# Kernel optimization log

Measured on AMD Instinct MI355X. Metric: run time of the kernel, lower is better.

Reference implementation:

```python
import jax, jax.numpy as jnp
import numpy as np

FEATURE_DIM = 1024
HEAD_NUM = 16
HIDDEN_DIM = FEATURE_DIM // HEAD_NUM


def setup_inputs() -> dict:
    key = jax.random.key(0)
    ks = jax.random.split(key, 12)
    B, S, D = 4, 2048, FEATURE_DIM
    s = 1.0 / np.sqrt(D)
    inp = {
        "query": jax.random.normal(ks[0], (B, S, D), jnp.float32),
        "key": jax.random.normal(ks[1], (B, S, D), jnp.float32),
        "value": jax.random.normal(ks[2], (B, S, D), jnp.float32),
        "mask": jax.random.randint(ks[3], (B, 1, 1, S), 0, 2, jnp.int32),
        "Wq": jax.random.normal(ks[4], (D, D), jnp.float32) * s,
        "bq": jnp.zeros((D,), jnp.float32),
        "Wk": jax.random.normal(ks[5], (D, D), jnp.float32) * s,
        "bk": jnp.zeros((D,), jnp.float32),
        "Wv": jax.random.normal(ks[6], (D, D), jnp.float32) * s,
        "bv": jnp.zeros((D,), jnp.float32),
        "Wo": jax.random.normal(ks[7], (D, D), jnp.float32) * s,
        "bo": jnp.zeros((D,), jnp.float32),
    }
    return inp


def reference(query, key, value, mask, Wq, bq, Wk, bk, Wv, bv, Wo, bo):
    B, Sq, D = query.shape
    H, Hd = HEAD_NUM, HIDDEN_DIM
    scale = jnp.sqrt(jnp.asarray(Hd, query.dtype))

    def split_heads(x):
        b, s, _ = x.shape
        return x.reshape(b, s, H, Hd).transpose(0, 2, 1, 3)  # [B,H,S,Hd]

    Q = split_heads(query @ Wq.T + bq)
    K = split_heads(key @ Wk.T + bk)
    V = split_heads(value @ Wv.T + bv)

    scores = jnp.einsum("bhqd,bhkd->bhqk", Q, K) / scale
    scores = jnp.where(mask == 0, jnp.asarray(-1e10, scores.dtype), scores)
    attn = jax.nn.softmax(scores, axis=-1)  # dropout p=0 -> identity
    h = jnp.einsum("bhqk,bhkd->bhqd", attn, V)
    h = h.transpose(0, 2, 1, 3).reshape(B, Sq, D)
    return h @ Wo.T + bo
```

## Files before the change

kernel.cpp:

```cpp
#include <hip/hip_runtime.h>
#include <hip/hip_bf16.h>
#include <cstdint>
#include <cstddef>

#define D_MODEL 1024
#define SEQ     2048
#define BATCH   4
#define NHEAD   16
#define HD      64
#define MROWS   (BATCH * SEQ)

typedef __attribute__((ext_vector_type(8))) short  short8;
typedef __attribute__((ext_vector_type(4))) float  floatx4;
typedef __attribute__((ext_vector_type(4))) unsigned short ushort4v;
typedef unsigned short u16;

__device__ __forceinline__ u16 f2bf(float x) {
    __hip_bfloat16 h = __float2bfloat16(x);
    return *(u16*)&h;
}

__device__ __forceinline__ void async_copy16(const u16* g, u16* l) {
    __builtin_amdgcn_global_load_lds(
        (const __attribute__((address_space(1))) void*)g,
        (__attribute__((address_space(3))) void*)l, 16, 0, 0);
}

__device__ __forceinline__ void cvt8(const float* s, u16* d, size_t i) {
    const float4 a = *(const float4*)(s + i);
    const float4 b = *(const float4*)(s + i + 4);
    short8 o;
    o[0] = (short)f2bf(a.x); o[1] = (short)f2bf(a.y);
    o[2] = (short)f2bf(a.z); o[3] = (short)f2bf(a.w);
    o[4] = (short)f2bf(b.x); o[5] = (short)f2bf(b.y);
    o[6] = (short)f2bf(b.z); o[7] = (short)f2bf(b.w);
    *(short8*)(d + i) = o;
}

__global__ __launch_bounds__(256) void cvt4(
    const float* __restrict__ s0, const float* __restrict__ s1,
    const float* __restrict__ s2, const float* __restrict__ s3,
    u16* __restrict__ d0, u16* __restrict__ d1,
    u16* __restrict__ d2, u16* __restrict__ d3)
{
    const float* s = blockIdx.y == 0 ? s0 : (blockIdx.y == 1 ? s1 :
                     (blockIdx.y == 2 ? s2 : s3));
    u16*         d = blockIdx.y == 0 ? d0 : (blockIdx.y == 1 ? d1 :
                     (blockIdx.y == 2 ? d2 : d3));
    cvt8(s, d, ((size_t)blockIdx.x * 256 + threadIdx.x) * 8);
}

__global__ __launch_bounds__(256) void gemm_qkv(
    const float* __restrict__ Aq, const float* __restrict__ Ak,
    const float* __restrict__ Av,
    const u16* __restrict__ Wqp, const u16* __restrict__ Wkp,
    const u16* __restrict__ Wvp,
    const float* __restrict__ bqp, const float* __restrict__ bkp,
    const float* __restrict__ bvp,
    u16* __restrict__ oq, u16* __restrict__ ok, u16* __restrict__ ov)
{
    constexpr int K = D_MODEL;
    __shared__ __align__(16) u16 smem[32768];

    const int z = blockIdx.z;
    const float* A    = z == 0 ? Aq  : (z == 1 ? Ak  : Av);
    const u16*   W    = z == 0 ? Wqp : (z == 1 ? Wkp : Wvp);
    const float* bias = z == 0 ? bqp : (z == 1 ? bkp : bvp);
    u16*         out  = z == 0 ? oq  : (z == 1 ? ok  : ov);

    const int bm = blockIdx.x * 128;
    const int bn = blockIdx.y * 128;
    const int t  = threadIdx.x;
    const int w  = t >> 6;
    const int l  = t & 63;
    const int li = l & 15;
    const int quad = l >> 4;
    const int wm = (w & 1) * 64;
    const int wn = (w >> 1) * 64;
    const int lrow = l >> 3;
    const int gch  = (l & 7) ^ lrow;
    const int swc  = gch * 8;
    const int rsw  = li & 7;
    const int srow = w * 32 + lrow;
    const int lc8  = (l & 7) * 8;

    const float* Ab = A + (size_t)bm * K;
    const u16*   Wg = W + (size_t)bn * K;

    float4 pa[4][2];

    floatx4 acc[4][4];
    #pragma unroll
    for (int mi = 0; mi < 4; mi++)
        #pragma unroll
        for (int ni = 0; ni < 4; ni++) acc[mi][ni] = (floatx4){0.f,0.f,0.f,0.f};

    #pragma unroll
    for (int j = 0; j < 4; j++) {
        const float* ap = Ab + (size_t)(srow + j * 8) * K + lc8;
        pa[j][0] = *(const float4*)ap;
        pa[j][1] = *(const float4*)(ap + 4);
    }
    #pragma unroll
    for (int j = 0; j < 4; j++) {
        const int r = w * 32 + j * 8;
        async_copy16(Wg + (size_t)(r + lrow) * K + gch * 8, smem + 8192 + r * 64);
    }
    #pragma unroll
    for (int j = 0; j < 4; j++) {
        short8 av;
        av[0] = (short)f2bf(pa[j][0].x); av[1] = (short)f2bf(pa[j][0].y);
        av[2] = (short)f2bf(pa[j][0].z); av[3] = (short)f2bf(pa[j][0].w);
        av[4] = (short)f2bf(pa[j][1].x); av[5] = (short)f2bf(pa[j][1].y);
        av[6] = (short)f2bf(pa[j][1].z); av[7] = (short)f2bf(pa[j][1].w);
        *(short8*)&smem[(srow + j * 8) * 64 + swc] = av;
    }

    int cur = 0;
    for (int kt = 0; kt < K; kt += 64) {
        __syncthreads();

        const bool pf = (kt + 64 < K);
        if (pf) {
            #pragma unroll
            for (int j = 0; j < 4; j++) {
                const float* ap = Ab + (size_t)(srow + j * 8) * K + kt + 64 + lc8;
                pa[j][0] = *(const float4*)ap;
                pa[j][1] = *(const float4*)(ap + 4);
            }
            u16* Wsn = smem + (cur ^ 1) * 16384 + 8192;
            #pragma unroll
            for (int j = 0; j < 4; j++) {
                const int r = w * 32 + j * 8;
                async_copy16(Wg + (size_t)(r + lrow) * K + kt + 64 + gch * 8, Wsn + r * 64);
            }
        }

        const u16* Asc = smem + cur * 16384;
        const u16* Wsc = Asc + 8192;
        #pragma unroll
        for (int ks = 0; ks < 2; ks++) {
            short8 af[4], bf[4];
            #pragma unroll
            for (int i = 0; i < 4; i++) {
                const int pc = ((ks * 4 + quad) ^ rsw) * 8;
                af[i] = *(const short8*)&Asc[(wm + i * 16 + li) * 64 + pc];
                bf[i] = *(const short8*)&Wsc[(wn + i * 16 + li) * 64 + pc];
            }
            #pragma unroll
            for (int mi = 0; mi < 4; mi++)
                #pragma unroll
                for (int ni = 0; ni < 4; ni++)
                    acc[mi][ni] = __builtin_amdgcn_mfma_f32_16x16x32_bf16(
                        af[mi], bf[ni], acc[mi][ni], 0, 0, 0);
        }

        if (pf) {
            u16* Asn = smem + (cur ^ 1) * 16384;
            #pragma unroll
            for (int j = 0; j < 4; j++) {
                short8 av;
                av[0] = (short)f2bf(pa[j][0].x); av[1] = (short)f2bf(pa[j][0].y);
                av[2] = (short)f2bf(pa[j][0].z); av[3] = (short)f2bf(pa[j][0].w);
                av[4] = (short)f2bf(pa[j][1].x); av[5] = (short)f2bf(pa[j][1].y);
                av[6] = (short)f2bf(pa[j][1].z); av[7] = (short)f2bf(pa[j][1].w);
                *(short8*)&Asn[(srow + j * 8) * 64 + swc] = av;
            }
        }
        cur ^= 1;
    }

    if (z < 2) {
        #pragma unroll
        for (int mi = 0; mi < 4; mi++)
            #pragma unroll
            for (int ni = 0; ni < 4; ni++) {
                const int c  = bn + wn + ni * 16 + li;
                const int h  = c >> 6;
                const int hd = c & 63;
                const float bz = bias[c];
                #pragma unroll
                for (int reg = 0; reg < 4; reg++) {
                    const int r = bm + wm + mi * 16 + quad * 4 + reg;
                    const int b = r >> 11;
                    const int s = r & (SEQ - 1);
                    out[(((size_t)(b * NHEAD + h) * SEQ) + s) * HD + hd] = f2bf(acc[mi][ni][reg] + bz);
                }
            }
    } else {
        u16 (*Ct)[128] = (u16(*)[128])smem;
        __syncthreads();
        #pragma unroll
        for (int mi = 0; mi < 4; mi++)
            #pragma unroll
            for (int ni = 0; ni < 4; ni++) {
                const int cl = wn + ni * 16 + li;
                const float bz = bias[bn + cl];
                #pragma unroll
                for (int reg = 0; reg < 4; reg++) {
                    const int rl = wm + mi * 16 + quad * 4 + reg;
                    Ct[cl][rl] = f2bf(acc[mi][ni][reg] + bz);
                }
            }
        __syncthreads();
        const int cl   = t >> 1;
        const int half = t & 1;
        const int cg = bn + cl;
        const int h  = cg >> 6;
        const int hd = cg & 63;
        const int b  = bm >> 11;
        const int s0 = (bm & (SEQ - 1)) + half * 64;
        u16* dst = out + (((size_t)(b * NHEAD + h) * HD) + hd) * SEQ + s0;
        const short8* sp = (const short8*)&Ct[cl][half * 64];
        #pragma unroll
        for (int i = 0; i < 8; i++) ((short8*)dst)[i] = sp[i];
    }
}

__global__ __launch_bounds__(256) void gemm_out(
    const u16* __restrict__ A,
    const u16* __restrict__ W,
    const float* __restrict__ bias,
    float* __restrict__ out)
{
    constexpr int K = D_MODEL;
    __shared__ __align__(16) u16 smem[32768];

    const int bm = blockIdx.x * 128;
    const int bn = blockIdx.y * 128;
    const int t  = threadIdx.x;
    const int w  = t >> 6;
    const int l  = t & 63;
    const int li = l & 15;
    const int quad = l >> 4;
    const int wm = (w & 1) * 64;
    const int wn = (w >> 1) * 64;
    const int lrow = l >> 3;
    const int gch  = (l & 7) ^ lrow;
    const int rsw  = li & 7;

    const u16* Ag = A + (size_t)bm * K;
    const u16* Wg = W + (size_t)bn * K;

    floatx4 acc[4][4];
    #pragma unroll
    for (int mi = 0; mi < 4; mi++)
        #pragma unroll
        for (int ni = 0; ni < 4; ni++) acc[mi][ni] = (floatx4){0.f,0.f,0.f,0.f};

    #pragma unroll
    for (int j = 0; j < 4; j++) {
        const int r = w * 32 + j * 8;
        async_copy16(Ag + (size_t)(r + lrow) * K + gch * 8, smem + r * 64);
        async_copy16(Wg + (size_t)(r + lrow) * K + gch * 8, smem + 8192 + r * 64);
    }

    int cur = 0;
    for (int kt = 0; kt < K; kt += 64) {
        __syncthreads();

        if (kt + 64 < K) {
            u16* Asn = smem + (cur ^ 1) * 16384;
            u16* Wsn = Asn + 8192;
            #pragma unroll
            for (int j = 0; j < 4; j++) {
                const int r = w * 32 + j * 8;
                async_copy16(Ag + (size_t)(r + lrow) * K + kt + 64 + gch * 8, Asn + r * 64);
                async_copy16(Wg + (size_t)(r + lrow) * K + kt + 64 + gch * 8, Wsn + r * 64);
            }
        }

        const u16* Asc = smem + cur * 16384;
        const u16* Wsc = Asc + 8192;
        #pragma unroll
        for (int ks = 0; ks < 2; ks++) {
            short8 af[4], bf[4];
            #pragma unroll
            for (int i = 0; i < 4; i++) {
                const int pc = ((ks * 4 + quad) ^ rsw) * 8;
                af[i] = *(const short8*)&Asc[(wm + i * 16 + li) * 64 + pc];
                bf[i] = *(const short8*)&Wsc[(wn + i * 16 + li) * 64 + pc];
            }
            #pragma unroll
            for (int mi = 0; mi < 4; mi++)
                #pragma unroll
                for (int ni = 0; ni < 4; ni++)
                    acc[mi][ni] = __builtin_amdgcn_mfma_f32_16x16x32_bf16(
                        af[mi], bf[ni], acc[mi][ni], 0, 0, 0);
        }
        cur ^= 1;
    }

    #pragma unroll
    for (int mi = 0; mi < 4; mi++)
        #pragma unroll
        for (int ni = 0; ni < 4; ni++) {
            const int c = bn + wn + ni * 16 + li;
            const float bz = bias[c];
            #pragma unroll
            for (int reg = 0; reg < 4; reg++) {
                const int r = bm + wm + mi * 16 + quad * 4 + reg;
                out[(size_t)r * D_MODEL + c] = acc[mi][ni][reg] + bz;
            }
        }
}

#define LOG2E   1.44269504088896340736f
#define CSCALE  (0.125f * LOG2E)

__global__ __launch_bounds__(256, 4) void attn_mfma(
    const u16* __restrict__ Q,
    const u16* __restrict__ K,
    const u16* __restrict__ Vt,
    const int* __restrict__ mask,
    u16* __restrict__ H)
{
    __shared__ __align__(16) u16 Ks[64 * 64];
    __shared__ __align__(16) u16 Vs[64 * 64];
    __shared__ __align__(16) u16 Ps[4][32][72];
    __shared__ __align__(16) float mc[64];

    const int bh  = blockIdx.y;
    const int b   = bh >> 4;
    const int h   = bh & 15;
    const int q0  = blockIdx.x * 128;
    const int t   = threadIdx.x;
    const int w   = t >> 6;
    const int l   = t & 63;
    const int li  = l & 15;
    const int quad  = l >> 4;
    const int lrow8 = l >> 3;
    const int gch   = (l & 7) ^ lrow8;
    const int swz   = li & 7;

    short8 qf[2][2];
    #pragma unroll
    for (int qb = 0; qb < 2; qb++) {
        const u16* Qrow = Q + ((size_t)bh * SEQ + q0 + w * 32 + qb * 16 + li) * HD;
        qf[qb][0] = *(const short8*)(Qrow + quad * 8);
        qf[qb][1] = *(const short8*)(Qrow + 32 + quad * 8);
    }

    const u16* Kbh = K  + (size_t)bh * SEQ * HD;
    const u16* Vbh = Vt + (size_t)bh * HD * SEQ;
    const int* mg  = mask + (size_t)b * SEQ;

    floatx4 oacc[4][2];
    #pragma unroll
    for (int hm = 0; hm < 4; hm++)
        #pragma unroll
        for (int qb = 0; qb < 2; qb++) oacc[hm][qb] = (floatx4){0.f,0.f,0.f,0.f};
    float rs[2] = {0.f, 0.f};

    #pragma unroll
    for (int j = 0; j < 2; j++) {
        const int rb = w * 16 + j * 8;
        async_copy16(Kbh + (size_t)(rb + lrow8) * HD + gch * 8, &Ks[rb * 64]);
    }
    if (t < 64) mc[t] = (mg[t] != 0) ? -16.0f : -1.0e9f;

    for (int kt = 0; kt < SEQ; kt += 64) {
        __syncthreads();

        #pragma unroll
        for (int j = 0; j < 2; j++) {
            const int rb = w * 16 + j * 8;
            async_copy16(Vbh + (size_t)(rb + lrow8) * SEQ + kt + gch * 8,
                         &Vs[rb * 64]);
        }

        #pragma unroll
        for (int kb = 0; kb < 4; kb++) {
            floatx4 s0 = (floatx4){0.f,0.f,0.f,0.f};
            floatx4 s1 = (floatx4){0.f,0.f,0.f,0.f};
            #pragma unroll
            for (int ks = 0; ks < 2; ks++) {
                const short8 kf = *(const short8*)
                    &Ks[(kb * 16 + li) * 64 + ((ks * 4 + quad) ^ swz) * 8];
                __builtin_amdgcn_s_setprio(1);
                s0 = __builtin_amdgcn_mfma_f32_16x16x32_bf16(kf, qf[0][ks], s0, 0, 0, 0);
                s1 = __builtin_amdgcn_mfma_f32_16x16x32_bf16(kf, qf[1][ks], s1, 0, 0, 0);
                __builtin_amdgcn_s_setprio(0);
            }
            const float4 m4 = *(const float4*)&mc[kb * 16 + quad * 4];
            {
                const float p0 = __builtin_amdgcn_exp2f(fmaf(s0[0], CSCALE, m4.x));
                const float p1 = __builtin_amdgcn_exp2f(fmaf(s0[1], CSCALE, m4.y));
                const float p2 = __builtin_amdgcn_exp2f(fmaf(s0[2], CSCALE, m4.z));
                const float p3 = __builtin_amdgcn_exp2f(fmaf(s0[3], CSCALE, m4.w));
                rs[0] += (p0 + p1) + (p2 + p3);
                ushort4v pk;
                pk[0] = f2bf(p0); pk[1] = f2bf(p1);
                pk[2] = f2bf(p2); pk[3] = f2bf(p3);
                *(ushort4v*)&Ps[w][li][kb * 16 + quad * 4] = pk;
            }
            {
                const float p0 = __builtin_amdgcn_exp2f(fmaf(s1[0], CSCALE, m4.x));
                const float p1 = __builtin_amdgcn_exp2f(fmaf(s1[1], CSCALE, m4.y));
                const float p2 = __builtin_amdgcn_exp2f(fmaf(s1[2], CSCALE, m4.z));
                const float p3 = __builtin_amdgcn_exp2f(fmaf(s1[3], CSCALE, m4.w));
                rs[1] += (p0 + p1) + (p2 + p3);
                ushort4v pk;
                pk[0] = f2bf(p0); pk[1] = f2bf(p1);
                pk[2] = f2bf(p2); pk[3] = f2bf(p3);
                *(ushort4v*)&Ps[w][16 + li][kb * 16 + quad * 4] = pk;
            }
        }

        __syncthreads();

        if (kt + 64 < SEQ) {
            #pragma unroll
            for (int j = 0; j < 2; j++) {
                const int rb = w * 16 + j * 8;
                async_copy16(Kbh + (size_t)(kt + 64 + rb + lrow8) * HD + gch * 8,
                             &Ks[rb * 64]);
            }
            if (t < 64) mc[t] = (mg[kt + 64 + t] != 0) ? -16.0f : -1.0e9f;
        }

        #pragma unroll
        for (int ks = 0; ks < 2; ks++) {
            short8 pf[2];
            #pragma unroll
            for (int qb = 0; qb < 2; qb++)
                pf[qb] = *(const short8*)&Ps[w][qb * 16 + li][ks * 32 + quad * 8];
            __builtin_amdgcn_s_setprio(1);
            #pragma unroll
            for (int hm = 0; hm < 4; hm++) {
                const short8 vf = *(const short8*)&Vs[(hm * 16 + li) * 64 + ((ks * 4 + quad) ^ swz) * 8];
                #pragma unroll
                for (int qb = 0; qb < 2; qb++)
                    oacc[hm][qb] = __builtin_amdgcn_mfma_f32_16x16x32_bf16(
                        vf, pf[qb], oacc[hm][qb], 0, 0, 0);
            }
            __builtin_amdgcn_s_setprio(0);
        }
    }

    float linv[2];
    #pragma unroll
    for (int qb = 0; qb < 2; qb++) {
        float v = rs[qb];
        v += __shfl_xor(v, 16, 64);
        v += __shfl_xor(v, 32, 64);
        linv[qb] = 1.0f / v;
    }
    #pragma unroll
    for (int qb = 0; qb < 2; qb++) {
        const size_t row = (size_t)b * SEQ + q0 + w * 32 + qb * 16 + li;
        #pragma unroll
        for (int hm = 0; hm < 4; hm++) {
            ushort4v o;
            #pragma unroll
            for (int reg = 0; reg < 4; reg++)
                o[reg] = f2bf(oacc[hm][qb][reg] * linv[qb]);
            *(ushort4v*)&H[row * D_MODEL + h * 64 + hm * 16 + quad * 4] = o;
        }
    }
}

extern "C" void kernel_launch(void* const* d_in, const int* in_sizes, int n_in,
                              void* d_out, int out_size, void* d_ws, size_t ws_size,
                              hipStream_t stream)
{
    const float* query = (const float*)d_in[0];
    const float* key_  = (const float*)d_in[1];
    const float* value = (const float*)d_in[2];
    const int*   mask  = (const int*)  d_in[3];
    const float* Wq = (const float*)d_in[4];
    const float* bq = (const float*)d_in[5];
    const float* Wk = (const float*)d_in[6];
    const float* bk = (const float*)d_in[7];
    const float* Wv = (const float*)d_in[8];
    const float* bv = (const float*)d_in[9];
    const float* Wo = (const float*)d_in[10];
    const float* bo = (const float*)d_in[11];
    float* out = (float*)d_out;

    const size_t per = (size_t)BATCH * NHEAD * SEQ * HD;
    const size_t wsz = (size_t)D_MODEL * D_MODEL;
    u16* Qb  = (u16*)d_ws;
    u16* Kb  = Qb  + per;
    u16* Vtb = Kb  + per;
    u16* Wqb = Vtb + per;
    u16* Wkb = Wqb + wsz;
    u16* Wvb = Wkb + wsz;
    u16* Wob = Wvb + wsz;
    u16* Hb  = Wob + wsz;

    cvt4<<<dim3(wsz / 2048, 4), 256, 0, stream>>>(Wq, Wk, Wv, Wo,
                                                  Wqb, Wkb, Wvb, Wob);

    gemm_qkv<<<dim3(MROWS / 128, D_MODEL / 128, 3), 256, 0, stream>>>(
        query, key_, value, Wqb, Wkb, Wvb, bq, bk, bv, Qb, Kb, Vtb);

    attn_mfma<<<dim3(SEQ / 128, BATCH * NHEAD), 256, 0, stream>>>(
        Qb, Kb, Vtb, mask, Hb);

    gemm_out<<<dim3(MROWS / 128, D_MODEL / 128), 256, 0, stream>>>(
        Hb, Wob, bo, out);
}
```

Baseline: 342.8 us.

## Load K, V and mask directly from global memory, dropping LDS staging and barriers

The attention kernel no longer stages K and V tiles and the mask in shared memory via async copies. Each wave now reads its K, V fragments and mask values straight from global memory (relying on L1/L2), which removes both __syncthreads per tile and frees LDS. The cost is that the four waves redundantly fetch the same K/V data from cache, and the software prefetch overlap is lost, so global load latency sits directly in front of the MFMAs.

```diff
diff --git a/kernel.cpp b/kernel.cpp
--- a/kernel.cpp
+++ b/kernel.cpp
@@ -315,10 +315,7 @@
     const int* __restrict__ mask,
     u16* __restrict__ H)
 {
-    __shared__ __align__(16) u16 Ks[64 * 64];
-    __shared__ __align__(16) u16 Vs[64 * 64];
     __shared__ __align__(16) u16 Ps[4][32][72];
-    __shared__ __align__(16) float mc[64];
 
     const int bh  = blockIdx.y;
     const int b   = bh >> 4;
@@ -328,10 +325,7 @@
     const int w   = t >> 6;
     const int l   = t & 63;
     const int li  = l & 15;
-    const int quad  = l >> 4;
-    const int lrow8 = l >> 3;
-    const int gch   = (l & 7) ^ lrow8;
-    const int swz   = li & 7;
+    const int quad = l >> 4;
 
     short8 qf[2][2];
     #pragma unroll
@@ -352,37 +346,26 @@
         for (int qb = 0; qb < 2; qb++) oacc[hm][qb] = (floatx4){0.f,0.f,0.f,0.f};
     float rs[2] = {0.f, 0.f};
 
-    #pragma unroll
-    for (int j = 0; j < 2; j++) {
-        const int rb = w * 16 + j * 8;
-        async_copy16(Kbh + (size_t)(rb + lrow8) * HD + gch * 8, &Ks[rb * 64]);
-    }
-    if (t < 64) mc[t] = (mg[t] != 0) ? -16.0f : -1.0e9f;
-
     for (int kt = 0; kt < SEQ; kt += 64) {
-        __syncthreads();
-
-        #pragma unroll
-        for (int j = 0; j < 2; j++) {
-            const int rb = w * 16 + j * 8;
-            async_copy16(Vbh + (size_t)(rb + lrow8) * SEQ + kt + gch * 8,
-                         &Vs[rb * 64]);
-        }
-
         #pragma unroll
         for (int kb = 0; kb < 4; kb++) {
             floatx4 s0 = (floatx4){0.f,0.f,0.f,0.f};
             floatx4 s1 = (floatx4){0.f,0.f,0.f,0.f};
+            const u16* Krow = Kbh + (size_t)(kt + kb * 16 + li) * HD;
             #pragma unroll
             for (int ks = 0; ks < 2; ks++) {
-                const short8 kf = *(const short8*)
-                    &Ks[(kb * 16 + li) * 64 + ((ks * 4 + quad) ^ swz) * 8];
+                const short8 kf = *(const short8*)(Krow + (ks * 4 + quad) * 8);
                 __builtin_amdgcn_s_setprio(1);
                 s0 = __builtin_amdgcn_mfma_f32_16x16x32_bf16(kf, qf[0][ks], s0, 0, 0, 0);
                 s1 = __builtin_amdgcn_mfma_f32_16x16x32_bf16(kf, qf[1][ks], s1, 0, 0, 0);
                 __builtin_amdgcn_s_setprio(0);
             }
-            const float4 m4 = *(const float4*)&mc[kb * 16 + quad * 4];
+            const int4 mi4 = *(const int4*)&mg[kt + kb * 16 + quad * 4];
+            float4 m4;
+            m4.x = (mi4.x != 0) ? -16.0f : -1.0e9f;
+            m4.y = (mi4.y != 0) ? -16.0f : -1.0e9f;
+            m4.z = (mi4.z != 0) ? -16.0f : -1.0e9f;
+            m4.w = (mi4.w != 0) ? -16.0f : -1.0e9f;
             {
                 const float p0 = __builtin_amdgcn_exp2f(fmaf(s0[0], CSCALE, m4.x));
                 const float p1 = __builtin_amdgcn_exp2f(fmaf(s0[1], CSCALE, m4.y));
@@ -407,34 +390,23 @@
             }
         }
 
-        __syncthreads();
-
-        if (kt + 64 < SEQ) {
-            #pragma unroll
-            for (int j = 0; j < 2; j++) {
-                const int rb = w * 16 + j * 8;
-                async_copy16(Kbh + (size_t)(kt + 64 + rb + lrow8) * HD + gch * 8,
-                             &Ks[rb * 64]);
-            }
-            if (t < 64) mc[t] = (mg[kt + 64 + t] != 0) ? -16.0f : -1.0e9f;
-        }
-
         #pragma unroll
         for (int ks = 0; ks < 2; ks++) {
             short8 pf[2];
             #pragma unroll
             for (int qb = 0; qb < 2; qb++)
                 pf[qb] = *(const short8*)&Ps[w][qb * 16 + li][ks * 32 + quad * 8];
-            __builtin_amdgcn_s_setprio(1);
             #pragma unroll
             for (int hm = 0; hm < 4; hm++) {
-                const short8 vf = *(const short8*)&Vs[(hm * 16 + li) * 64 + ((ks * 4 + quad) ^ swz) * 8];
+                const short8 vf = *(const short8*)
+                    (Vbh + (size_t)(hm * 16 + li) * SEQ + kt + (ks * 4 + quad) * 8);
+                __builtin_amdgcn_s_setprio(1);
                 #pragma unroll
                 for (int qb = 0; qb < 2; qb++)
                     oacc[hm][qb] = __builtin_amdgcn_mfma_f32_16x16x32_bf16(
                         vf, pf[qb], oacc[hm][qb], 0, 0, 0);
-            }
-            __builtin_amdgcn_s_setprio(0);
+                __builtin_amdgcn_s_setprio(0);
+            }
         }
     }
 
```

Measured after the change: 501.9 us. 46.4% more time.
